# Performance work log

Hardware: AMD Instinct MI355X
Metric: run time of the kernel (lower is better)

## Reference

```python
import jax, jax.numpy as jnp
import numpy as np

H, KVH, DH = 32, 8, 128      # n query heads, n kv heads, head dim
LN_EPS = 1e-5
ROPE_THETA = 10000.0


def setup_inputs() -> dict:
    key = jax.random.key(0)
    ks = jax.random.split(key, 4)
    B, T, D = 2, 4096, 4096
    scale = 0.02
    return {
        "x": jax.random.normal(ks[0], (B, T, D), dtype=jnp.float32),
        "gamma": jnp.ones((D,), dtype=jnp.float32),
        "beta": jnp.zeros((D,), dtype=jnp.float32),
        "Wq": jax.random.normal(ks[1], (D, H * DH), dtype=jnp.float32) * scale,
        "Wk": jax.random.normal(ks[2], (D, KVH * DH), dtype=jnp.float32) * scale,
        "Wv": jax.random.normal(ks[3], (D, KVH * DH), dtype=jnp.float32) * scale,
    }


def _rope(u, cos, sin):
    # rotate-half RoPE; u: [B, T, h, DH]
    half = DH // 2
    rot = jnp.concatenate([-u[..., half:], u[..., :half]], axis=-1)
    return u * cos + rot * sin


def reference(x, gamma, beta, Wq, Wk, Wv):
    B, T, D = x.shape
    # LayerNorm
    mu = jnp.mean(x, axis=-1, keepdims=True)
    xc = x - mu
    var = jnp.mean(xc * xc, axis=-1, keepdims=True)
    x_ln = xc * jax.lax.rsqrt(var + LN_EPS) * gamma + beta

    # fused QKV projection + head split
    q = (x_ln @ Wq).reshape(B, T, H, DH)
    k = (x_ln @ Wk).reshape(B, T, KVH, DH)
    v = (x_ln @ Wv).reshape(B, T, KVH, DH)

    # RoPE with position_ids = arange(T) (default path)
    pos = jnp.arange(T, dtype=jnp.float32)
    inv_freq = 1.0 / (ROPE_THETA ** (jnp.arange(0, DH, 2, dtype=jnp.float32) / DH))
    ang = pos[:, None] * inv_freq                      # [T, DH/2]
    cos = jnp.concatenate([jnp.cos(ang)] * 2, axis=-1)[None, :, None, :]  # [1,T,1,DH]
    sin = jnp.concatenate([jnp.sin(ang)] * 2, axis=-1)[None, :, None, :]
    q = _rope(q, cos, sin)
    k = _rope(k, cos, sin)

    # transpose to [B, h, T, DH]
    queries = jnp.swapaxes(q, 1, 2)
    keys = jnp.swapaxes(k, 1, 2)
    values = jnp.swapaxes(v, 1, 2)

    # GQA expansion: each kv head repeated expansion times (grouped), matching
    # unsqueeze(2).expand(...).flatten(1,2)
    expansion = H // KVH
    keys_e = jnp.repeat(keys, expansion, axis=1)
    values_e = jnp.repeat(values, expansion, axis=1)
    return queries, keys_e, values_e
```

## Files before the change

### kernel.cpp

```cpp
#include <hip/hip_runtime.h>
#include <cstdint>
#include <cstddef>

typedef unsigned short u16;
typedef unsigned int u32;
using f32x4  = __attribute__((ext_vector_type(4))) float;
using bf16x8 = __attribute__((ext_vector_type(8))) __bf16;

#define D_  4096
#define NC_ 6144
#define NQ_ 4096
#define NK_ 1024
#define H_  32
#define T_  4096
#define DH_ 128

__device__ __forceinline__ float bf2f(u16 h) {
  u32 u = ((u32)h) << 16;
  return __builtin_bit_cast(float, u);
}
__device__ __forceinline__ u16 f2bf(float f) {
  u32 u = __builtin_bit_cast(u32, f);
  u = u + 0x7FFFu + ((u >> 16) & 1u);
  return (u16)(u >> 16);
}

__global__ void detect_kernel(const u32* gamma_bits, int* flag) {
  if (threadIdx.x == 0) flag[0] = (gamma_bits[0] == 0x3F803F80u) ? 1 : 0;
}

__global__ __launch_bounds__(256) void ln_kernel(const void* xv, const void* gv, const void* bv,
                                                 u16* __restrict__ xln, const int* flag) {
  const bool bf = (*flag != 0);
  const int r = blockIdx.x;
  const int t = threadIdx.x;
  const size_t base = (size_t)r * D_;
  float vals[16];
  if (bf) {
    const u16* x = (const u16*)xv;
    #pragma unroll
    for (int i = 0; i < 2; ++i) {
      const int cc = i * 2048 + t * 8;
      uint4 q = *(const uint4*)(x + base + cc);
      u32 w[4] = {q.x, q.y, q.z, q.w};
      #pragma unroll
      for (int j = 0; j < 8; ++j)
        vals[i * 8 + j] = bf2f((u16)(w[j >> 1] >> ((j & 1) * 16)));
    }
  } else {
    const float* x = (const float*)xv;
    #pragma unroll
    for (int i = 0; i < 2; ++i) {
      const int cc = i * 2048 + t * 8;
      float4 a  = *(const float4*)(x + base + cc);
      float4 b2 = *(const float4*)(x + base + cc + 4);
      vals[i*8+0] = a.x;  vals[i*8+1] = a.y;  vals[i*8+2] = a.z;  vals[i*8+3] = a.w;
      vals[i*8+4] = b2.x; vals[i*8+5] = b2.y; vals[i*8+6] = b2.z; vals[i*8+7] = b2.w;
    }
  }
  float s = 0.f, sq = 0.f;
  #pragma unroll
  for (int j = 0; j < 16; ++j) { s += vals[j]; sq += vals[j] * vals[j]; }
  #pragma unroll
  for (int off = 32; off > 0; off >>= 1) {
    s  += __shfl_xor(s, off, 64);
    sq += __shfl_xor(sq, off, 64);
  }
  __shared__ float redS[4], redQ[4], mrs[2];
  const int wave = t >> 6, lane = t & 63;
  if (lane == 0) { redS[wave] = s; redQ[wave] = sq; }
  __syncthreads();
  if (t == 0) {
    float S = redS[0] + redS[1] + redS[2] + redS[3];
    float Q = redQ[0] + redQ[1] + redQ[2] + redQ[3];
    float mu = S * (1.0f / D_);
    float var = Q * (1.0f / D_) - mu * mu;
    mrs[0] = mu;
    mrs[1] = rsqrtf(var + 1e-5f);
  }
  __syncthreads();
  const float mu = mrs[0], rs = mrs[1];
  #pragma unroll
  for (int i = 0; i < 2; ++i) {
    const int cc = i * 2048 + t * 8;
    float g[8], be[8];
    if (bf) {
      const u16* gp = (const u16*)gv;
      const u16* bp = (const u16*)bv;
      uint4 qg = *(const uint4*)(gp + cc);
      uint4 qb = *(const uint4*)(bp + cc);
      u32 wg[4] = {qg.x, qg.y, qg.z, qg.w};
      u32 wb[4] = {qb.x, qb.y, qb.z, qb.w};
      #pragma unroll
      for (int j = 0; j < 8; ++j) {
        g[j]  = bf2f((u16)(wg[j >> 1] >> ((j & 1) * 16)));
        be[j] = bf2f((u16)(wb[j >> 1] >> ((j & 1) * 16)));
      }
    } else {
      const float* gp = (const float*)gv;
      const float* bp = (const float*)bv;
      float4 a  = *(const float4*)(gp + cc);
      float4 b2 = *(const float4*)(gp + cc + 4);
      float4 c  = *(const float4*)(bp + cc);
      float4 d2 = *(const float4*)(bp + cc + 4);
      g[0]=a.x; g[1]=a.y; g[2]=a.z; g[3]=a.w; g[4]=b2.x; g[5]=b2.y; g[6]=b2.z; g[7]=b2.w;
      be[0]=c.x; be[1]=c.y; be[2]=c.z; be[3]=c.w; be[4]=d2.x; be[5]=d2.y; be[6]=d2.z; be[7]=d2.w;
    }
    u32 o[4];
    #pragma unroll
    for (int j = 0; j < 4; ++j) {
      u16 lo = f2bf((vals[i*8 + j*2    ] - mu) * rs * g[j*2    ] + be[j*2    ]);
      u16 hi = f2bf((vals[i*8 + j*2 + 1] - mu) * rs * g[j*2 + 1] + be[j*2 + 1]);
      o[j] = (u32)lo | ((u32)hi << 16);
    }
    *(uint4*)(xln + base + cc) = make_uint4(o[0], o[1], o[2], o[3]);
  }
}

__global__ __launch_bounds__(256) void wt_kernel(const void* wq, const void* wk, const void* wv,
                                                 u16* __restrict__ wt, const int* flag) {
  const bool bf = (*flag != 0);
  __shared__ u16 tile[64 * 66];
  int bid = blockIdx.x;
  const void* src; int N, nbase;
  if (bid < 4096)      { src = wq; N = 4096; nbase = 0; }
  else if (bid < 5120) { src = wk; N = 1024; nbase = 4096; bid -= 4096; }
  else                 { src = wv; N = 1024; nbase = 5120; bid -= 5120; }
  const int kt = bid & 63, nt = bid >> 6;
  const int k0 = kt << 6, n0 = nt << 6;
  const int t = threadIdx.x;
  if (bf) {
    const u16* sp = (const u16*)src;
    const int klr = t >> 3, kl8 = t & 7;
    #pragma unroll
    for (int it = 0; it < 2; ++it) {
      const int kr = it * 32 + klr;
      uint4 q = *(const uint4*)(sp + (size_t)(k0 + kr) * N + n0 + kl8 * 8);
      u32 w[4] = {q.x, q.y, q.z, q.w};
      #pragma unroll
      for (int j = 0; j < 8; ++j)
        tile[kr * 66 + kl8 * 8 + j] = (u16)(w[j >> 1] >> ((j & 1) * 16));
    }
  } else {
    const float* sp = (const float*)src;
    const int klr = t >> 4, kl16 = t & 15;
    #pragma unroll
    for (int it = 0; it < 4; ++it) {
      const int kr = it * 16 + klr;
      float4 f = *(const float4*)(sp + (size_t)(k0 + kr) * N + n0 + kl16 * 4);
      tile[kr * 66 + kl16 * 4 + 0] = f2bf(f.x);
      tile[kr * 66 + kl16 * 4 + 1] = f2bf(f.y);
      tile[kr * 66 + kl16 * 4 + 2] = f2bf(f.z);
      tile[kr * 66 + kl16 * 4 + 3] = f2bf(f.w);
    }
  }
  __syncthreads();
  const int wlr = t >> 3, wl8 = t & 7;
  #pragma unroll
  for (int it = 0; it < 2; ++it) {
    const int nr = it * 32 + wlr;
    u32 o[4];
    #pragma unroll
    for (int j = 0; j < 4; ++j) {
      u16 lo = tile[(wl8 * 8 + j * 2    ) * 66 + nr];
      u16 hi = tile[(wl8 * 8 + j * 2 + 1) * 66 + nr];
      o[j] = (u32)lo | ((u32)hi << 16);
    }
    *(uint4*)(wt + (size_t)(nbase + n0 + nr) * 4096 + k0 + wl8 * 8) = make_uint4(o[0], o[1], o[2], o[3]);
  }
}

#define STAGE_A(tk, buf, r) \
  __builtin_amdgcn_global_load_lds((__attribute__((address_space(1))) u32*)(A + (size_t)(m0 + (r)*64 + srow) * 4096 + (size_t)(tk) + scol), \
      (__attribute__((address_space(3))) u32*)&lA[buf][(r)*4096 + wbase], 16, 0, 0)
#define STAGE_B(tk, buf, r) \
  __builtin_amdgcn_global_load_lds((__attribute__((address_space(1))) u32*)(Bm + (size_t)(n0 + (r)*64 + srow) * 4096 + (size_t)(tk) + scol), \
      (__attribute__((address_space(3))) u32*)&lB[buf][(r)*4096 + wbase], 16, 0, 0)
#define LDA(dst, buf, mi, kk) do { const int r_ = wm + (mi)*16 + l15; \
  (dst) = *(const bf16x8*)&lA[buf][r_*64 + ((((kk)*4 + quad) ^ (r_ & 7)) << 3)]; } while (0)
#define LDB(dst, buf, ni, kk) do { const int r_ = wn + (ni)*16 + l15; \
  (dst) = *(const bf16x8*)&lB[buf][r_*64 + ((((kk)*4 + quad) ^ (r_ & 7)) << 3)]; } while (0)
#define MFMA_(a, b, c) (c) = __builtin_amdgcn_mfma_f32_16x16x32_bf16((a), (b), (c), 0, 0, 0)

#define KTILE(BUFC, BUFN, KT) do { \
  bf16x8 a0[4][2], a1[4][2], b0[2][2], b1[2][2]; \
   \
  asm volatile("s_waitcnt vmcnt(4)" ::: "memory"); \
  __builtin_amdgcn_s_barrier(); \
  _Pragma("unroll") for (int mi = 0; mi < 4; ++mi) { LDA(a0[mi][0], BUFC, mi, 0); LDA(a0[mi][1], BUFC, mi, 1); } \
  _Pragma("unroll") for (int ni = 0; ni < 2; ++ni) { LDB(b0[ni][0], BUFC, ni, 0); LDB(b0[ni][1], BUFC, ni, 1); } \
  STAGE_A((KT) + 64, BUFN, 0); STAGE_A((KT) + 64, BUFN, 1); \
  __builtin_amdgcn_s_barrier(); \
  asm volatile("s_waitcnt lgkmcnt(0)" ::: "memory"); \
  __builtin_amdgcn_s_setprio(1); \
  _Pragma("unroll") for (int mi = 0; mi < 4; ++mi) _Pragma("unroll") for (int ni = 0; ni < 2; ++ni) { \
    MFMA_(a0[mi][0], b0[ni][0], acc[mi][ni]); MFMA_(a0[mi][1], b0[ni][1], acc[mi][ni]); } \
  __builtin_amdgcn_s_setprio(0); \
   \
  _Pragma("unroll") for (int ni = 0; ni < 2; ++ni) { LDB(b1[ni][0], BUFC, ni + 2, 0); LDB(b1[ni][1], BUFC, ni + 2, 1); } \
  STAGE_A((KT) + 64, BUFN, 2); STAGE_A((KT) + 64, BUFN, 3); \
  __builtin_amdgcn_s_barrier(); \
  asm volatile("s_waitcnt lgkmcnt(0)" ::: "memory"); \
  __builtin_amdgcn_s_setprio(1); \
  _Pragma("unroll") for (int mi = 0; mi < 4; ++mi) _Pragma("unroll") for (int ni = 0; ni < 2; ++ni) { \
    MFMA_(a0[mi][0], b1[ni][0], acc[mi][ni + 2]); MFMA_(a0[mi][1], b1[ni][1], acc[mi][ni + 2]); } \
  __builtin_amdgcn_s_setprio(0); \
   \
  _Pragma("unroll") for (int mi = 0; mi < 4; ++mi) { LDA(a1[mi][0], BUFC, mi + 4, 0); LDA(a1[mi][1], BUFC, mi + 4, 1); } \
  STAGE_B((KT) + 128, BUFC, 0); STAGE_B((KT) + 128, BUFC, 1); \
  __builtin_amdgcn_s_barrier(); \
  asm volatile("s_waitcnt lgkmcnt(0)" ::: "memory"); \
  __builtin_amdgcn_s_setprio(1); \
  _Pragma("unroll") for (int mi = 0; mi < 4; ++mi) _Pragma("unroll") for (int ni = 0; ni < 2; ++ni) { \
    MFMA_(a1[mi][0], b0[ni][0], acc[mi + 4][ni]); MFMA_(a1[mi][1], b0[ni][1], acc[mi + 4][ni]); } \
  __builtin_amdgcn_s_setprio(0); \
   \
  STAGE_B((KT) + 128, BUFC, 2); STAGE_B((KT) + 128, BUFC, 3); \
  __builtin_amdgcn_s_barrier(); \
  __builtin_amdgcn_s_setprio(1); \
  _Pragma("unroll") for (int mi = 0; mi < 4; ++mi) _Pragma("unroll") for (int ni = 0; ni < 2; ++ni) { \
    MFMA_(a1[mi][0], b1[ni][0], acc[mi + 4][ni + 2]); MFMA_(a1[mi][1], b1[ni][1], acc[mi + 4][ni + 2]); } \
  __builtin_amdgcn_s_setprio(0); \
} while (0)

__global__ __launch_bounds__(512, 1) void gemm_kernel(const u16* __restrict__ A,
                                                      const u16* __restrict__ Bm,
                                                      u16* __restrict__ Cm) {
  __shared__ u16 lA[2][16384];
  __shared__ u16 lB[2][16384];

  int wg = blockIdx.x;
  wg = (wg & 7) * 96 + (wg >> 3);
  const int m0 = (wg & 31) * 256;
  const int n0 = (wg >> 5) * 256;

  const int t = threadIdx.x;
  const int lane = t & 63, wave = t >> 6;
  const int wm = (wave >> 2) * 128;
  const int wn = (wave & 3) * 64;
  const int l15 = lane & 15, quad = lane >> 4;

  const int srow = t >> 3;
  const int scol = (((t & 7) ^ (srow & 7)) << 3);
  const int wbase = wave * 512;

  f32x4 acc[8][4];
  #pragma unroll
  for (int mi = 0; mi < 8; ++mi)
    #pragma unroll
    for (int ni = 0; ni < 4; ++ni)
      acc[mi][ni] = (f32x4){0.f, 0.f, 0.f, 0.f};

  #pragma unroll
  for (int r = 0; r < 4; ++r) STAGE_A(0, 0, r);
  #pragma unroll
  for (int r = 0; r < 4; ++r) STAGE_B(0, 0, r);
  #pragma unroll
  for (int r = 0; r < 4; ++r) STAGE_B(64, 1, r);

  for (int kt = 0; kt < 4096; kt += 128) {
    KTILE(0, 1, kt);
    KTILE(1, 0, kt + 64);
  }
  asm volatile("s_waitcnt vmcnt(0)" ::: "memory");

  #pragma unroll
  for (int mi = 0; mi < 8; ++mi) {
    const int rowb = m0 + wm + mi * 16 + quad * 4;
    #pragma unroll
    for (int ni = 0; ni < 4; ++ni) {
      const int col = n0 + wn + ni * 16 + l15;
      #pragma unroll
      for (int rr = 0; rr < 4; ++rr)
        Cm[(size_t)(rowb + rr) * NC_ + col] = f2bf(acc[mi][ni][rr]);
    }
  }
}

__global__ __launch_bounds__(256) void rope_kernel(const u16* __restrict__ Cm, void* outv,
                                                   const int* flag) {
  const bool obf = (*flag != 0);
  const int r = blockIdx.x;
  const int t = threadIdx.x;
  const int b = r >> 12;
  const int tp = r & 4095;
  const size_t cbase = (size_t)r * NC_;
  const int d = t & 63;
  const int grp = t >> 6;
  const float invf = exp2f(-0.20762050593046014f * (float)d);
  const float ang = (float)tp * invf;
  const float s = sinf(ang);
  const float c = cosf(ang);
  u16* ob = (u16*)outv;
  float* of = (float*)outv;
  const size_t QS = (size_t)2 * H_ * T_ * DH_;

  #pragma unroll
  for (int j = 0; j < 8; ++j) {
    const int h = grp * 8 + j;
    const float u0 = bf2f(Cm[cbase + h * 128 + d]);
    const float u1 = bf2f(Cm[cbase + h * 128 + 64 + d]);
    const float o0 = u0 * c - u1 * s;
    const float o1 = u1 * c + u0 * s;
    const size_t o = ((size_t)(b * H_ + h) * T_ + tp) * DH_ + d;
    if (obf) { ob[o] = f2bf(o0); ob[o + 64] = f2bf(o1); }
    else     { of[o] = o0;       of[o + 64] = o1; }
  }
  #pragma unroll
  for (int j = 0; j < 2; ++j) {
    const int g = grp * 2 + j;
    const float u0 = bf2f(Cm[cbase + NQ_ + g * 128 + d]);
    const float u1 = bf2f(Cm[cbase + NQ_ + g * 128 + 64 + d]);
    const float o0 = u0 * c - u1 * s;
    const float o1 = u1 * c + u0 * s;
    #pragma unroll
    for (int e = 0; e < 4; ++e) {
      const int h = g * 4 + e;
      const size_t o = QS + ((size_t)(b * H_ + h) * T_ + tp) * DH_ + d;
      if (obf) { ob[o] = f2bf(o0); ob[o + 64] = f2bf(o1); }
      else     { of[o] = o0;       of[o + 64] = o1; }
    }
  }
  #pragma unroll
  for (int j = 0; j < 4; ++j) {
    const int idx = j * 256 + t;
    const int g = idx >> 7, dd = idx & 127;
    const u16 raw = Cm[cbase + NQ_ + NK_ + g * 128 + dd];
    const float fv = bf2f(raw);
    #pragma unroll
    for (int e = 0; e < 4; ++e) {
      const int h = g * 4 + e;
      const size_t o = 2 * QS + ((size_t)(b * H_ + h) * T_ + tp) * DH_ + dd;
      if (obf) ob[o] = raw; else of[o] = fv;
    }
  }
}

extern "C" void kernel_launch(void* const* d_in, const int* in_sizes, int n_in,
                              void* d_out, int out_size, void* d_ws, size_t ws_size,
                              hipStream_t stream) {
  const void* x  = d_in[0];
  const void* g  = d_in[1];
  const void* be = d_in[2];
  const void* wq = d_in[3];
  const void* wk = d_in[4];
  const void* wv = d_in[5];
  char* ws = (char*)d_ws;
  int* flag = (int*)ws;
  u16* xln  = (u16*)(ws + 256);
  u16* wt   = (u16*)(ws + 256 + 67108864);
  u16* Cm   = (u16*)(ws + 256 + 67108864 + 50331648);

  detect_kernel<<<1, 64, 0, stream>>>((const u32*)g, flag);
  ln_kernel<<<8192, 256, 0, stream>>>(x, g, be, xln, flag);
  wt_kernel<<<6144, 256, 0, stream>>>(wq, wk, wv, wt, flag);
  gemm_kernel<<<dim3(768), 512, 0, stream>>>(xln, wt, Cm);
  rope_kernel<<<8192, 256, 0, stream>>>(Cm, d_out, flag);
}
```

Measured before the change: 987.5 us.

## Rebalance GEMM LDS staging order and vectorize RoPE loads/stores

The GEMM K-tile loop reorders its global-to-LDS staging so that each phase issues a mix of A and B tile rows, with the prologue changed to match. The goal is to spread prefetch traffic more evenly between MFMA phases. The RoPE/scatter kernel now handles two adjacent elements per thread with 32-bit loads and stores for Q/K and four elements with 64/128-bit accesses for V, cutting the number of memory instructions. The staging reorder depends on which LDS regions are already consumed at each barrier, so a mistake there would be a data race.

```diff
diff --git a/kernel.cpp b/kernel.cpp
--- a/kernel.cpp
+++ b/kernel.cpp
@@ -189,7 +189,8 @@
   __builtin_amdgcn_s_barrier(); \
   _Pragma("unroll") for (int mi = 0; mi < 4; ++mi) { LDA(a0[mi][0], BUFC, mi, 0); LDA(a0[mi][1], BUFC, mi, 1); } \
   _Pragma("unroll") for (int ni = 0; ni < 2; ++ni) { LDB(b0[ni][0], BUFC, ni, 0); LDB(b0[ni][1], BUFC, ni, 1); } \
-  STAGE_A((KT) + 64, BUFN, 0); STAGE_A((KT) + 64, BUFN, 1); \
+  STAGE_A((KT) + 64, BUFN, 1); STAGE_A((KT) + 64, BUFN, 3); \
+  STAGE_B((KT) + 64, BUFN, 2); STAGE_B((KT) + 64, BUFN, 3); \
   __builtin_amdgcn_s_barrier(); \
   asm volatile("s_waitcnt lgkmcnt(0)" ::: "memory"); \
   __builtin_amdgcn_s_setprio(1); \
@@ -198,7 +199,6 @@
   __builtin_amdgcn_s_setprio(0); \
    \
   _Pragma("unroll") for (int ni = 0; ni < 2; ++ni) { LDB(b1[ni][0], BUFC, ni + 2, 0); LDB(b1[ni][1], BUFC, ni + 2, 1); } \
-  STAGE_A((KT) + 64, BUFN, 2); STAGE_A((KT) + 64, BUFN, 3); \
   __builtin_amdgcn_s_barrier(); \
   asm volatile("s_waitcnt lgkmcnt(0)" ::: "memory"); \
   __builtin_amdgcn_s_setprio(1); \
@@ -207,7 +207,7 @@
   __builtin_amdgcn_s_setprio(0); \
    \
   _Pragma("unroll") for (int mi = 0; mi < 4; ++mi) { LDA(a1[mi][0], BUFC, mi + 4, 0); LDA(a1[mi][1], BUFC, mi + 4, 1); } \
-  STAGE_B((KT) + 128, BUFC, 0); STAGE_B((KT) + 128, BUFC, 1); \
+  STAGE_A((KT) + 128, BUFC, 0); STAGE_A((KT) + 128, BUFC, 2); \
   __builtin_amdgcn_s_barrier(); \
   asm volatile("s_waitcnt lgkmcnt(0)" ::: "memory"); \
   __builtin_amdgcn_s_setprio(1); \
@@ -215,7 +215,7 @@
     MFMA_(a1[mi][0], b0[ni][0], acc[mi + 4][ni]); MFMA_(a1[mi][1], b0[ni][1], acc[mi + 4][ni]); } \
   __builtin_amdgcn_s_setprio(0); \
    \
-  STAGE_B((KT) + 128, BUFC, 2); STAGE_B((KT) + 128, BUFC, 3); \
+  STAGE_B((KT) + 128, BUFC, 0); STAGE_B((KT) + 128, BUFC, 1); \
   __builtin_amdgcn_s_barrier(); \
   __builtin_amdgcn_s_setprio(1); \
   _Pragma("unroll") for (int mi = 0; mi < 4; ++mi) _Pragma("unroll") for (int ni = 0; ni < 2; ++ni) { \
@@ -255,8 +255,8 @@
   for (int r = 0; r < 4; ++r) STAGE_A(0, 0, r);
   #pragma unroll
   for (int r = 0; r < 4; ++r) STAGE_B(0, 0, r);
-  #pragma unroll
-  for (int r = 0; r < 4; ++r) STAGE_B(64, 1, r);
+  STAGE_A(64, 1, 0); STAGE_A(64, 1, 2);
+  STAGE_B(64, 1, 0); STAGE_B(64, 1, 1);
 
   for (int kt = 0; kt < 4096; kt += 128) {
     KTILE(0, 1, kt);
@@ -285,53 +285,72 @@
   const int b = r >> 12;
   const int tp = r & 4095;
   const size_t cbase = (size_t)r * NC_;
-  const int d = t & 63;
-  const int grp = t >> 6;
-  const float invf = exp2f(-0.20762050593046014f * (float)d);
-  const float ang = (float)tp * invf;
-  const float s = sinf(ang);
-  const float c = cosf(ang);
+  const int p = t & 31;
+  const int g8 = t >> 5;
+  const int d0 = 2 * p;
+  const float k2 = -0.20762050593046014f;
+  const float invf0 = exp2f(k2 * (float)d0);
+  const float invf1 = exp2f(k2 * (float)(d0 + 1));
+  const float a0 = (float)tp * invf0, a1 = (float)tp * invf1;
+  const float s0 = sinf(a0), c0 = cosf(a0);
+  const float s1 = sinf(a1), c1 = cosf(a1);
   u16* ob = (u16*)outv;
   float* of = (float*)outv;
   const size_t QS = (size_t)2 * H_ * T_ * DH_;
 
   #pragma unroll
-  for (int j = 0; j < 8; ++j) {
-    const int h = grp * 8 + j;
-    const float u0 = bf2f(Cm[cbase + h * 128 + d]);
-    const float u1 = bf2f(Cm[cbase + h * 128 + 64 + d]);
-    const float o0 = u0 * c - u1 * s;
-    const float o1 = u1 * c + u0 * s;
-    const size_t o = ((size_t)(b * H_ + h) * T_ + tp) * DH_ + d;
-    if (obf) { ob[o] = f2bf(o0); ob[o + 64] = f2bf(o1); }
-    else     { of[o] = o0;       of[o + 64] = o1; }
-  }
-  #pragma unroll
-  for (int j = 0; j < 2; ++j) {
-    const int g = grp * 2 + j;
-    const float u0 = bf2f(Cm[cbase + NQ_ + g * 128 + d]);
-    const float u1 = bf2f(Cm[cbase + NQ_ + g * 128 + 64 + d]);
-    const float o0 = u0 * c - u1 * s;
-    const float o1 = u1 * c + u0 * s;
+  for (int j = 0; j < 4; ++j) {
+    const int h = j * 8 + g8;
+    const u32 w0 = *(const u32*)&Cm[cbase + h * 128 + d0];
+    const u32 w1 = *(const u32*)&Cm[cbase + h * 128 + 64 + d0];
+    const float u0a = bf2f((u16)w0), u0b = bf2f((u16)(w0 >> 16));
+    const float u1a = bf2f((u16)w1), u1b = bf2f((u16)(w1 >> 16));
+    const float o0a = u0a * c0 - u1a * s0, o0b = u0b * c1 - u1b * s1;
+    const float o1a = u1a * c0 + u0a * s0, o1b = u1b * c1 + u0b * s1;
+    const size_t o = ((size_t)(b * H_ + h) * T_ + tp) * DH_ + d0;
+    if (obf) {
+      *(u32*)(ob + o)      = (u32)f2bf(o0a) | ((u32)f2bf(o0b) << 16);
+      *(u32*)(ob + o + 64) = (u32)f2bf(o1a) | ((u32)f2bf(o1b) << 16);
+    } else {
+      *(float2*)(of + o)      = make_float2(o0a, o0b);
+      *(float2*)(of + o + 64) = make_float2(o1a, o1b);
+    }
+  }
+  {
+    const int g = g8;
+    const u32 w0 = *(const u32*)&Cm[cbase + NQ_ + g * 128 + d0];
+    const u32 w1 = *(const u32*)&Cm[cbase + NQ_ + g * 128 + 64 + d0];
+    const float u0a = bf2f((u16)w0), u0b = bf2f((u16)(w0 >> 16));
+    const float u1a = bf2f((u16)w1), u1b = bf2f((u16)(w1 >> 16));
+    const float o0a = u0a * c0 - u1a * s0, o0b = u0b * c1 - u1b * s1;
+    const float o1a = u1a * c0 + u0a * s0, o1b = u1b * c1 + u0b * s1;
+    const u32 pk0 = (u32)f2bf(o0a) | ((u32)f2bf(o0b) << 16);
+    const u32 pk1 = (u32)f2bf(o1a) | ((u32)f2bf(o1b) << 16);
     #pragma unroll
     for (int e = 0; e < 4; ++e) {
       const int h = g * 4 + e;
-      const size_t o = QS + ((size_t)(b * H_ + h) * T_ + tp) * DH_ + d;
-      if (obf) { ob[o] = f2bf(o0); ob[o + 64] = f2bf(o1); }
-      else     { of[o] = o0;       of[o + 64] = o1; }
-    }
-  }
-  #pragma unroll
-  for (int j = 0; j < 4; ++j) {
-    const int idx = j * 256 + t;
-    const int g = idx >> 7, dd = idx & 127;
-    const u16 raw = Cm[cbase + NQ_ + NK_ + g * 128 + dd];
-    const float fv = bf2f(raw);
+      const size_t o = QS + ((size_t)(b * H_ + h) * T_ + tp) * DH_ + d0;
+      if (obf) {
+        *(u32*)(ob + o)      = pk0;
+        *(u32*)(ob + o + 64) = pk1;
+      } else {
+        *(float2*)(of + o)      = make_float2(o0a, o0b);
+        *(float2*)(of + o + 64) = make_float2(o1a, o1b);
+      }
+    }
+  }
+  {
+    const int g = g8;
+    const int dd = 4 * p;
+    const uint2 w = *(const uint2*)&Cm[cbase + NQ_ + NK_ + g * 128 + dd];
+    const float v0 = bf2f((u16)w.x), v1 = bf2f((u16)(w.x >> 16));
+    const float v2 = bf2f((u16)w.y), v3 = bf2f((u16)(w.y >> 16));
     #pragma unroll
     for (int e = 0; e < 4; ++e) {
       const int h = g * 4 + e;
       const size_t o = 2 * QS + ((size_t)(b * H_ + h) * T_ + tp) * DH_ + dd;
-      if (obf) ob[o] = raw; else of[o] = fv;
+      if (obf) *(uint2*)(ob + o) = w;
+      else     *(float4*)(of + o) = make_float4(v0, v1, v2, v3);
     }
   }
 }
```

New measurement: 950.2 us. -3.8%, faster.
